# Kernel optimization log

Hardware: AMD Instinct MI355X
Metric: run time of the kernel (lower is better)

## Reference

```python
import jax, jax.numpy as jnp
import numpy as np

N = 100000   # nodes
D = 64       # in_features
E = 1200000  # edges (avg degree ~12)
C = 1.0      # curvature
MIN_NORM = 1e-15
PROJ_EPS = 4e-3  # float32 eps used by HGCN-style PoincareBall.proj


def setup_inputs() -> dict:
    key = jax.random.key(0)
    k1, k2, k3 = jax.random.split(key, 3)
    x = jax.random.normal(k1, (N, D), dtype=jnp.float32) * 0.1
    edge_index = jax.random.randint(k2, (2, E), 0, N, dtype=jnp.int32)
    # GCNConv learned params (lin weight + bias)
    W = jax.random.normal(k3, (D, D), dtype=jnp.float32) / np.sqrt(D)
    b = jnp.zeros((D,), dtype=jnp.float32)
    return {"x": x, "W": W, "b": b, "edge_index": edge_index}


def expmap0(u, c):
    sqrt_c = jnp.sqrt(c)
    u_norm = jnp.maximum(jnp.linalg.norm(u, axis=-1, keepdims=True), MIN_NORM)
    return jnp.tanh(sqrt_c * u_norm) * u / (sqrt_c * u_norm)


def proj(x, c):
    norm = jnp.maximum(jnp.linalg.norm(x, axis=-1, keepdims=True), MIN_NORM)
    maxnorm = (1.0 - PROJ_EPS) / jnp.sqrt(c)
    return jnp.where(norm > maxnorm, x / norm * maxnorm, x)


def gcn_conv(x, W, b, edge_index, n_nodes):
    # PyG GCNConv: h = x @ W; add self-loops; symmetric normalization; scatter-add; + bias
    h = x @ W  # [N, D]
    src, dst = edge_index[0], edge_index[1]
    loops = jnp.arange(n_nodes, dtype=edge_index.dtype)
    s = jnp.concatenate([src, loops])  # [E+N]
    d = jnp.concatenate([dst, loops])
    deg = jax.ops.segment_sum(jnp.ones(s.shape, dtype=h.dtype), d, num_segments=n_nodes)
    deg_inv_sqrt = jnp.where(deg > 0, deg ** -0.5, 0.0)
    norm = deg_inv_sqrt[s] * deg_inv_sqrt[d]  # [E+N]
    msgs = h[s] * norm[:, None]               # gather + scale: [E+N, D]
    out = jax.ops.segment_sum(msgs, d, num_segments=n_nodes)  # scatter-add
    return out + b


def reference(x, W, b, edge_index):
    # Note: original computes logmap0(x) but discards it (conv uses raw x) -- dead code.
    support_t = gcn_conv(x, W, b, edge_index, N)
    return proj(expmap0(support_t, C), C)
```

## Files before the change

kernel.cpp:

```cpp
#include <hip/hip_runtime.h>
#include <hip/hip_bf16.h>

#define DFEAT 64
#define NBSH  8
#define NPB   256
#define EPB   4096
#define EPT   (EPB / 256)
#define CAPB  3584
#define REGS  4608
#define BSTR  32

__global__ __launch_bounds__(256) void part_kernel(const int* __restrict__ ei,
                                                   int* __restrict__ bcnt,
                                                   unsigned* __restrict__ ebuf, int E) {
    __shared__ int h[512];
    __shared__ int base[512];
    int t = threadIdx.x;
    h[t] = 0; h[t + 256] = 0;
    __syncthreads();
    int bb = blockIdx.x * EPB;
    int sv[EPT], dv[EPT];
    #pragma unroll
    for (int i = 0; i < EPT; ++i) {
        int e = bb + i * 256 + t;
        if (e < E) {
            sv[i] = ei[e];
            dv[i] = ei[E + e];
            atomicAdd(&h[dv[i] >> NBSH], 1);
        } else dv[i] = -1;
    }
    __syncthreads();
    base[t]       = h[t]       ? atomicAdd(&bcnt[t * BSTR],         h[t])       : 0;
    base[t + 256] = h[t + 256] ? atomicAdd(&bcnt[(t + 256) * BSTR], h[t + 256]) : 0;
    __syncthreads();
    h[t] = 0; h[t + 256] = 0;
    __syncthreads();
    #pragma unroll
    for (int i = 0; i < EPT; ++i) {
        if (dv[i] >= 0) {
            int bkt = dv[i] >> NBSH;
            int pos = base[bkt] + atomicAdd(&h[bkt], 1);
            if (pos < CAPB)
                ebuf[(size_t)bkt * REGS + pos] =
                    (unsigned)sv[i] | ((unsigned)(dv[i] & (NPB - 1)) << 17);
        }
    }
}

__global__ __launch_bounds__(256) void csr_kernel(const int* __restrict__ bcnt,
                                                  unsigned* __restrict__ buf,
                                                  int2* __restrict__ bl,
                                                  float* __restrict__ dinv, int n) {
    __shared__ unsigned eb[CAPB];
    __shared__ int cnt[256];
    __shared__ int tmp[256];
    int t = threadIdx.x, b = blockIdx.x;
    int ecnt = bcnt[b * BSTR]; if (ecnt > CAPB) ecnt = CAPB;
    size_t rb = (size_t)b * REGS;

    const uint4* bufv = (const uint4*)(buf + rb);
    uint4* ebv = (uint4*)eb;
    int nv = (ecnt + 3) >> 2;
    for (int i = t; i < nv; i += 256) ebv[i] = bufv[i];
    cnt[t] = 0;
    __syncthreads();
    for (int i = t; i < ecnt; i += 256) atomicAdd(&cnt[eb[i] >> 17], 1);
    __syncthreads();

    int nid = (b << NBSH) + t;
    int deg = cnt[t];
    int slots = (nid < n) ? ((deg + 4) & ~3) : 0;
    tmp[t] = slots;
    __syncthreads();
    int s = slots;
    for (int o = 1; o < 256; o <<= 1) {
        int y = (t >= o) ? tmp[t - o] : 0;
        __syncthreads();
        tmp[t] += y;
        __syncthreads();
    }
    int excl = tmp[t] - s;
    int beg = (int)rb + excl;
    if (nid < n) {
        bl[nid] = make_int2(beg, slots);
        dinv[nid] = rsqrtf((float)(deg + 1));
        buf[beg] = (unsigned)nid;
        for (int k = deg + 1; k < slots; ++k) buf[beg + k] = (unsigned)n;
    }
    cnt[t] = excl + 1;
    __syncthreads();
    for (int i = t; i < ecnt; i += 256) {
        unsigned v = eb[i];
        int pos = atomicAdd(&cnt[v >> 17], 1);
        buf[rb + pos] = v & 0x1ffffu;
    }
}

__global__ __launch_bounds__(256) void xsprep_kernel(const float* __restrict__ x,
                                                     const float* __restrict__ dinv,
                                                     unsigned* __restrict__ xs, int n) {
    int i = blockIdx.x * blockDim.x + threadIdx.x;
    int total = (n + 1) * 32;
    if (i >= total) return;
    int row = i >> 5, col = i & 31;
    unsigned v = 0;
    if (row < n) {
        float di = dinv[row];
        float f0 = x[(size_t)row * DFEAT + 2 * col] * di;
        float f1 = x[(size_t)row * DFEAT + 2 * col + 1] * di;
        unsigned u0 = __float_as_uint(f0); u0 = (u0 + 0x7fffu + ((u0 >> 16) & 1u)) >> 16;
        unsigned u1 = __float_as_uint(f1); u1 = (u1 + 0x7fffu + ((u1 >> 16) & 1u)) >> 16;
        v = (u0 & 0xffffu) | (u1 << 16);
    }
    xs[i] = v;
}

__global__ __launch_bounds__(256) void agg_kernel(const int2* __restrict__ bl,
                                                  const int* __restrict__ srcs,
                                                  const float* __restrict__ dinv,
                                                  const uint2* __restrict__ xs2,
                                                  const float* __restrict__ W,
                                                  const float* __restrict__ b,
                                                  float* __restrict__ out,
                                                  int n, int octbase, int octend) {
    __shared__ float Wl[DFEAT * DFEAT];
    __shared__ float xl[8][DFEAT];
    int t = threadIdx.x;
    #pragma unroll
    for (int i = 0; i < 16; ++i) Wl[i * 256 + t] = W[i * 256 + t];
    __syncthreads();

    int r = t >> 6, lane = t & 63;
    int g = lane >> 4;
    int q = lane & 15;
    float bias = b[lane];

    for (int oct = octbase + blockIdx.x; oct < octend; oct += gridDim.x) {
        int na = oct * 8 + r;
        int nb_ = na + 4;
        bool va = na < n, vb = nb_ < n;
        if (!va) continue;

        int2 p0 = bl[na];
        int beg0 = p0.x, end0 = p0.x + p0.y;
        int beg1 = 0, end1 = 0;
        if (vb) { int2 p1 = bl[nb_]; beg1 = p1.x; end1 = p1.x + p1.y; }

        float a0 = 0, a1 = 0, a2 = 0, a3 = 0;
        float b0 = 0, b1 = 0, b2 = 0, b3 = 0;
        int base0 = beg0, base1 = beg1;
        while (base0 < end0 || base1 < end1) {
            int m0 = end0 - base0; m0 = m0 < 0 ? 0 : (m0 > 64 ? 64 : m0);
            int m1 = end1 - base1; m1 = m1 < 0 ? 0 : (m1 > 64 ? 64 : m1);
            int idx0 = 0, idx1 = 0;
            if (lane < m0) idx0 = srcs[base0 + lane];
            if (lane < m1) idx1 = srcs[base1 + lane];
            int q0 = m0 >> 2, q1 = m1 >> 2;
            int qc = q0 < q1 ? q0 : q1;
            #pragma unroll 4
            for (int j = 0; j < qc; ++j) {
                int sv0 = __shfl(idx0, 4 * j + g, 64);
                int sv1 = __shfl(idx1, 4 * j + g, 64);
                uint2 d0 = xs2[(unsigned)sv0 * 16 + q];
                uint2 d1 = xs2[(unsigned)sv1 * 16 + q];
                a0 += __uint_as_float(d0.x << 16);
                a1 += __uint_as_float(d0.x & 0xffff0000u);
                a2 += __uint_as_float(d0.y << 16);
                a3 += __uint_as_float(d0.y & 0xffff0000u);
                b0 += __uint_as_float(d1.x << 16);
                b1 += __uint_as_float(d1.x & 0xffff0000u);
                b2 += __uint_as_float(d1.y << 16);
                b3 += __uint_as_float(d1.y & 0xffff0000u);
            }
            #pragma unroll 4
            for (int j = qc; j < q0; ++j) {
                int sv0 = __shfl(idx0, 4 * j + g, 64);
                uint2 d0 = xs2[(unsigned)sv0 * 16 + q];
                a0 += __uint_as_float(d0.x << 16);
                a1 += __uint_as_float(d0.x & 0xffff0000u);
                a2 += __uint_as_float(d0.y << 16);
                a3 += __uint_as_float(d0.y & 0xffff0000u);
            }
            #pragma unroll 4
            for (int j = qc; j < q1; ++j) {
                int sv1 = __shfl(idx1, 4 * j + g, 64);
                uint2 d1 = xs2[(unsigned)sv1 * 16 + q];
                b0 += __uint_as_float(d1.x << 16);
                b1 += __uint_as_float(d1.x & 0xffff0000u);
                b2 += __uint_as_float(d1.y << 16);
                b3 += __uint_as_float(d1.y & 0xffff0000u);
            }
            base0 += 64; base1 += 64;
        }
        #pragma unroll
        for (int off = 16; off < 64; off <<= 1) {
            a0 += __shfl_xor(a0, off, 64);
            a1 += __shfl_xor(a1, off, 64);
            a2 += __shfl_xor(a2, off, 64);
            a3 += __shfl_xor(a3, off, 64);
            b0 += __shfl_xor(b0, off, 64);
            b1 += __shfl_xor(b1, off, 64);
            b2 += __shfl_xor(b2, off, 64);
            b3 += __shfl_xor(b3, off, 64);
        }
        if (g == 0) {
            float dia = dinv[na];
            xl[r][4 * q + 0] = a0 * dia;
            xl[r][4 * q + 1] = a1 * dia;
            xl[r][4 * q + 2] = a2 * dia;
            xl[r][4 * q + 3] = a3 * dia;
            if (vb) {
                float dib = dinv[nb_];
                xl[r + 4][4 * q + 0] = b0 * dib;
                xl[r + 4][4 * q + 1] = b1 * dib;
                xl[r + 4][4 * q + 2] = b2 * dib;
                xl[r + 4][4 * q + 3] = b3 * dib;
            }
        }

        float oa0 = bias, oa1 = 0.0f, ob0 = bias, ob1 = 0.0f;
        #pragma unroll
        for (int k = 0; k < DFEAT; k += 2) {
            float w0 = Wl[k * DFEAT + lane];
            float w1 = Wl[(k + 1) * DFEAT + lane];
            oa0 = fmaf(xl[r][k],     w0, oa0);
            oa1 = fmaf(xl[r][k + 1], w1, oa1);
            ob0 = fmaf(xl[r + 4][k],     w0, ob0);
            ob1 = fmaf(xl[r + 4][k + 1], w1, ob1);
        }
        float oa = oa0 + oa1;
        float ob = ob0 + ob1;

        float ssa = oa * oa, ssb = ob * ob;
        #pragma unroll
        for (int off = 32; off > 0; off >>= 1) {
            ssa += __shfl_xor(ssa, off, 64);
            ssb += __shfl_xor(ssb, off, 64);
        }
        float norma = fmaxf(sqrtf(ssa), 1e-15f);
        float sca = fminf(tanhf(norma), 1.0f - 4e-3f) / norma;
        out[(long long)na * DFEAT + lane] = oa * sca;
        if (vb) {
            float normb = fmaxf(sqrtf(ssb), 1e-15f);
            float scb = fminf(tanhf(normb), 1.0f - 4e-3f) / normb;
            out[(long long)nb_ * DFEAT + lane] = ob * scb;
        }
    }
}


extern "C" void kernel_launch(void* const* d_in, const int* in_sizes, int n_in,
                              void* d_out, int out_size, void* d_ws, size_t ws_size,
                              hipStream_t stream) {
    const float* x = (const float*)d_in[0];
    const float* W = (const float*)d_in[1];
    const float* b = (const float*)d_in[2];
    const int* ei  = (const int*)d_in[3];

    int n = in_sizes[0] / DFEAT;
    int E = in_sizes[3] / 2;
    int NBUCK = (n + NPB - 1) / NPB;
    int nblk = (E + EPB - 1) / EPB;
    int noctets = (n + 7) / 8;

    int* bcnt = (int*)d_ws;
    unsigned* buf = (unsigned*)(bcnt + 512 * BSTR);
    int2* bl = (int2*)(buf + (size_t)NBUCK * REGS);
    float* dinv = (float*)(bl + n);
    size_t xsoff = (size_t)(((int*)dinv + n) - (int*)d_ws);
    xsoff = (xsoff + 31) & ~(size_t)31;
    unsigned* xs = (unsigned*)d_ws + xsoff;

    float* out = (float*)d_out;

    int xsblocks = ((n + 1) * 32 + 255) / 256;

    hipMemsetAsync(bcnt, 0, 512 * BSTR * sizeof(int), stream);
    part_kernel  <<<nblk, 256, 0, stream>>>(ei, bcnt, buf, E);
    csr_kernel   <<<NBUCK, 256, 0, stream>>>(bcnt, buf, bl, dinv, n);
    xsprep_kernel<<<xsblocks, 256, 0, stream>>>(x, dinv, xs, n);

    int Q = (noctets + 3) / 4;
    for (int qd = 0; qd < 4; ++qd) {
        int ob = qd * Q;
        int oe = ob + Q; if (oe > noctets) oe = noctets;
        if (ob >= oe) break;
        int blks = oe - ob; if (blks > 2048) blks = 2048;
        agg_kernel<<<blks, 256, 0, stream>>>(bl, (const int*)buf, dinv,
                                             (const uint2*)xs, W, b, out, n, ob, oe);
    }
}
```

Baseline: 192.1 us.

## Fuse partition, CSR build, feature prep and aggregation into one cooperative kernel

```diff
diff --git a/kernel.cpp b/kernel.cpp
--- a/kernel.cpp
+++ b/kernel.cpp
@@ -1,5 +1,7 @@
 #include <hip/hip_runtime.h>
-#include <hip/hip_bf16.h>
+#include <hip/hip_cooperative_groups.h>
+
+namespace cg = cooperative_groups;
 
 #define DFEAT 64
 #define NBSH  8
@@ -9,241 +11,248 @@
 #define CAPB  3584
 #define REGS  4608
 #define BSTR  32
-
-__global__ __launch_bounds__(256) void part_kernel(const int* __restrict__ ei,
-                                                   int* __restrict__ bcnt,
-                                                   unsigned* __restrict__ ebuf, int E) {
-    __shared__ int h[512];
-    __shared__ int base[512];
+#define GRID  1024
+
+__global__ __launch_bounds__(256, 4) void mega_kernel(
+    const int* __restrict__ ei, const float* __restrict__ x,
+    const float* __restrict__ W, const float* __restrict__ bias_,
+    int* __restrict__ bcnt, unsigned* __restrict__ buf,
+    int2* __restrict__ bl, float* __restrict__ dinv,
+    unsigned* __restrict__ xs, float* __restrict__ out,
+    int n, int E, int nblk, int nbuck, int noctets)
+{
+    cg::grid_group grid = cg::this_grid();
+    __shared__ __align__(16) unsigned char smem[18432];
     int t = threadIdx.x;
-    h[t] = 0; h[t + 256] = 0;
-    __syncthreads();
-    int bb = blockIdx.x * EPB;
-    int sv[EPT], dv[EPT];
-    #pragma unroll
-    for (int i = 0; i < EPT; ++i) {
-        int e = bb + i * 256 + t;
-        if (e < E) {
-            sv[i] = ei[e];
-            dv[i] = ei[E + e];
-            atomicAdd(&h[dv[i] >> NBSH], 1);
-        } else dv[i] = -1;
-    }
-    __syncthreads();
-    base[t]       = h[t]       ? atomicAdd(&bcnt[t * BSTR],         h[t])       : 0;
-    base[t + 256] = h[t + 256] ? atomicAdd(&bcnt[(t + 256) * BSTR], h[t + 256]) : 0;
-    __syncthreads();
-    h[t] = 0; h[t + 256] = 0;
-    __syncthreads();
-    #pragma unroll
-    for (int i = 0; i < EPT; ++i) {
-        if (dv[i] >= 0) {
-            int bkt = dv[i] >> NBSH;
-            int pos = base[bkt] + atomicAdd(&h[bkt], 1);
-            if (pos < CAPB)
-                ebuf[(size_t)bkt * REGS + pos] =
-                    (unsigned)sv[i] | ((unsigned)(dv[i] & (NPB - 1)) << 17);
-        }
-    }
-}
-
-__global__ __launch_bounds__(256) void csr_kernel(const int* __restrict__ bcnt,
-                                                  unsigned* __restrict__ buf,
-                                                  int2* __restrict__ bl,
-                                                  float* __restrict__ dinv, int n) {
-    __shared__ unsigned eb[CAPB];
-    __shared__ int cnt[256];
-    __shared__ int tmp[256];
-    int t = threadIdx.x, b = blockIdx.x;
-    int ecnt = bcnt[b * BSTR]; if (ecnt > CAPB) ecnt = CAPB;
-    size_t rb = (size_t)b * REGS;
-
-    const uint4* bufv = (const uint4*)(buf + rb);
-    uint4* ebv = (uint4*)eb;
-    int nv = (ecnt + 3) >> 2;
-    for (int i = t; i < nv; i += 256) ebv[i] = bufv[i];
-    cnt[t] = 0;
-    __syncthreads();
-    for (int i = t; i < ecnt; i += 256) atomicAdd(&cnt[eb[i] >> 17], 1);
-    __syncthreads();
-
-    int nid = (b << NBSH) + t;
-    int deg = cnt[t];
-    int slots = (nid < n) ? ((deg + 4) & ~3) : 0;
-    tmp[t] = slots;
-    __syncthreads();
-    int s = slots;
-    for (int o = 1; o < 256; o <<= 1) {
-        int y = (t >= o) ? tmp[t - o] : 0;
-        __syncthreads();
-        tmp[t] += y;
-        __syncthreads();
-    }
-    int excl = tmp[t] - s;
-    int beg = (int)rb + excl;
-    if (nid < n) {
-        bl[nid] = make_int2(beg, slots);
-        dinv[nid] = rsqrtf((float)(deg + 1));
-        buf[beg] = (unsigned)nid;
-        for (int k = deg + 1; k < slots; ++k) buf[beg + k] = (unsigned)n;
-    }
-    cnt[t] = excl + 1;
-    __syncthreads();
-    for (int i = t; i < ecnt; i += 256) {
-        unsigned v = eb[i];
-        int pos = atomicAdd(&cnt[v >> 17], 1);
-        buf[rb + pos] = v & 0x1ffffu;
-    }
-}
-
-__global__ __launch_bounds__(256) void xsprep_kernel(const float* __restrict__ x,
-                                                     const float* __restrict__ dinv,
-                                                     unsigned* __restrict__ xs, int n) {
-    int i = blockIdx.x * blockDim.x + threadIdx.x;
-    int total = (n + 1) * 32;
-    if (i >= total) return;
-    int row = i >> 5, col = i & 31;
-    unsigned v = 0;
-    if (row < n) {
-        float di = dinv[row];
-        float f0 = x[(size_t)row * DFEAT + 2 * col] * di;
-        float f1 = x[(size_t)row * DFEAT + 2 * col + 1] * di;
-        unsigned u0 = __float_as_uint(f0); u0 = (u0 + 0x7fffu + ((u0 >> 16) & 1u)) >> 16;
-        unsigned u1 = __float_as_uint(f1); u1 = (u1 + 0x7fffu + ((u1 >> 16) & 1u)) >> 16;
-        v = (u0 & 0xffffu) | (u1 << 16);
-    }
-    xs[i] = v;
-}
-
-__global__ __launch_bounds__(256) void agg_kernel(const int2* __restrict__ bl,
-                                                  const int* __restrict__ srcs,
-                                                  const float* __restrict__ dinv,
-                                                  const uint2* __restrict__ xs2,
-                                                  const float* __restrict__ W,
-                                                  const float* __restrict__ b,
-                                                  float* __restrict__ out,
-                                                  int n, int octbase, int octend) {
-    __shared__ float Wl[DFEAT * DFEAT];
-    __shared__ float xl[8][DFEAT];
-    int t = threadIdx.x;
-    #pragma unroll
-    for (int i = 0; i < 16; ++i) Wl[i * 256 + t] = W[i * 256 + t];
-    __syncthreads();
-
-    int r = t >> 6, lane = t & 63;
-    int g = lane >> 4;
-    int q = lane & 15;
-    float bias = b[lane];
-
-    for (int oct = octbase + blockIdx.x; oct < octend; oct += gridDim.x) {
-        int na = oct * 8 + r;
-        int nb_ = na + 4;
-        bool va = na < n, vb = nb_ < n;
-        if (!va) continue;
-
-        int2 p0 = bl[na];
-        int beg0 = p0.x, end0 = p0.x + p0.y;
-        int beg1 = 0, end1 = 0;
-        if (vb) { int2 p1 = bl[nb_]; beg1 = p1.x; end1 = p1.x + p1.y; }
-
-        float a0 = 0, a1 = 0, a2 = 0, a3 = 0;
-        float b0 = 0, b1 = 0, b2 = 0, b3 = 0;
-        int base0 = beg0, base1 = beg1;
-        while (base0 < end0 || base1 < end1) {
-            int m0 = end0 - base0; m0 = m0 < 0 ? 0 : (m0 > 64 ? 64 : m0);
-            int m1 = end1 - base1; m1 = m1 < 0 ? 0 : (m1 > 64 ? 64 : m1);
-            int idx0 = 0, idx1 = 0;
-            if (lane < m0) idx0 = srcs[base0 + lane];
-            if (lane < m1) idx1 = srcs[base1 + lane];
-            int q0 = m0 >> 2, q1 = m1 >> 2;
-            int qc = q0 < q1 ? q0 : q1;
-            #pragma unroll 4
-            for (int j = 0; j < qc; ++j) {
-                int sv0 = __shfl(idx0, 4 * j + g, 64);
-                int sv1 = __shfl(idx1, 4 * j + g, 64);
-                uint2 d0 = xs2[(unsigned)sv0 * 16 + q];
-                uint2 d1 = xs2[(unsigned)sv1 * 16 + q];
-                a0 += __uint_as_float(d0.x << 16);
-                a1 += __uint_as_float(d0.x & 0xffff0000u);
-                a2 += __uint_as_float(d0.y << 16);
-                a3 += __uint_as_float(d0.y & 0xffff0000u);
-                b0 += __uint_as_float(d1.x << 16);
-                b1 += __uint_as_float(d1.x & 0xffff0000u);
-                b2 += __uint_as_float(d1.y << 16);
-                b3 += __uint_as_float(d1.y & 0xffff0000u);
-            }
-            #pragma unroll 4
-            for (int j = qc; j < q0; ++j) {
-                int sv0 = __shfl(idx0, 4 * j + g, 64);
-                uint2 d0 = xs2[(unsigned)sv0 * 16 + q];
-                a0 += __uint_as_float(d0.x << 16);
-                a1 += __uint_as_float(d0.x & 0xffff0000u);
-                a2 += __uint_as_float(d0.y << 16);
-                a3 += __uint_as_float(d0.y & 0xffff0000u);
-            }
-            #pragma unroll 4
-            for (int j = qc; j < q1; ++j) {
-                int sv1 = __shfl(idx1, 4 * j + g, 64);
-                uint2 d1 = xs2[(unsigned)sv1 * 16 + q];
-                b0 += __uint_as_float(d1.x << 16);
-                b1 += __uint_as_float(d1.x & 0xffff0000u);
-                b2 += __uint_as_float(d1.y << 16);
-                b3 += __uint_as_float(d1.y & 0xffff0000u);
-            }
-            base0 += 64; base1 += 64;
-        }
+    int bid = blockIdx.x;
+
+    for (int i = bid * 256 + t; i < 512 * BSTR; i += GRID * 256) bcnt[i] = 0;
+    grid.sync();
+
+    if (bid < nblk) {
+        int* h    = (int*)smem;
+        int* base = h + 512;
+        h[t] = 0; h[t + 256] = 0;
+        __syncthreads();
+        int bb = bid * EPB;
+        int sv[EPT], dv[EPT];
         #pragma unroll
-        for (int off = 16; off < 64; off <<= 1) {
-            a0 += __shfl_xor(a0, off, 64);
-            a1 += __shfl_xor(a1, off, 64);
-            a2 += __shfl_xor(a2, off, 64);
-            a3 += __shfl_xor(a3, off, 64);
-            b0 += __shfl_xor(b0, off, 64);
-            b1 += __shfl_xor(b1, off, 64);
-            b2 += __shfl_xor(b2, off, 64);
-            b3 += __shfl_xor(b3, off, 64);
-        }
-        if (g == 0) {
-            float dia = dinv[na];
-            xl[r][4 * q + 0] = a0 * dia;
-            xl[r][4 * q + 1] = a1 * dia;
-            xl[r][4 * q + 2] = a2 * dia;
-            xl[r][4 * q + 3] = a3 * dia;
+        for (int i = 0; i < EPT; ++i) {
+            int e = bb + i * 256 + t;
+            if (e < E) {
+                sv[i] = ei[e];
+                dv[i] = ei[E + e];
+                atomicAdd(&h[dv[i] >> NBSH], 1);
+            } else dv[i] = -1;
+        }
+        __syncthreads();
+        base[t]       = h[t]       ? atomicAdd(&bcnt[t * BSTR],         h[t])       : 0;
+        base[t + 256] = h[t + 256] ? atomicAdd(&bcnt[(t + 256) * BSTR], h[t + 256]) : 0;
+        __syncthreads();
+        h[t] = 0; h[t + 256] = 0;
+        __syncthreads();
+        #pragma unroll
+        for (int i = 0; i < EPT; ++i) {
+            if (dv[i] >= 0) {
+                int bkt = dv[i] >> NBSH;
+                int pos = base[bkt] + atomicAdd(&h[bkt], 1);
+                if (pos < CAPB)
+                    buf[(size_t)bkt * REGS + pos] =
+                        (unsigned)sv[i] | ((unsigned)(dv[i] & (NPB - 1)) << 17);
+            }
+        }
+    }
+    grid.sync();
+
+    if (bid < nbuck) {
+        unsigned* eb = (unsigned*)smem;
+        int* cnt = (int*)(smem + CAPB * 4);
+        int* tmp = cnt + 256;
+        int b = bid;
+        int ecnt = bcnt[b * BSTR]; if (ecnt > CAPB) ecnt = CAPB;
+        size_t rb = (size_t)b * REGS;
+
+        const uint4* bufv = (const uint4*)(buf + rb);
+        uint4* ebv = (uint4*)eb;
+        int nv = (ecnt + 3) >> 2;
+        for (int i = t; i < nv; i += 256) ebv[i] = bufv[i];
+        cnt[t] = 0;
+        __syncthreads();
+        for (int i = t; i < ecnt; i += 256) atomicAdd(&cnt[eb[i] >> 17], 1);
+        __syncthreads();
+
+        int nid = (b << NBSH) + t;
+        int deg = cnt[t];
+        int slots = (nid < n) ? ((deg + 4) & ~3) : 0;
+        tmp[t] = slots;
+        __syncthreads();
+        int s = slots;
+        for (int o = 1; o < 256; o <<= 1) {
+            int y = (t >= o) ? tmp[t - o] : 0;
+            __syncthreads();
+            tmp[t] += y;
+            __syncthreads();
+        }
+        int excl = tmp[t] - s;
+        int beg = (int)rb + excl;
+        if (nid < n) {
+            bl[nid] = make_int2(beg, slots);
+            dinv[nid] = rsqrtf((float)(deg + 1));
+            buf[beg] = (unsigned)nid;
+            for (int k = deg + 1; k < slots; ++k) buf[beg + k] = (unsigned)n;
+        }
+        cnt[t] = excl + 1;
+        __syncthreads();
+        for (int i = t; i < ecnt; i += 256) {
+            unsigned v = eb[i];
+            int pos = atomicAdd(&cnt[v >> 17], 1);
+            buf[rb + pos] = v & 0x1ffffu;
+        }
+    }
+    grid.sync();
+
+    {
+        int total = (n + 1) * 32;
+        for (int i = bid * 256 + t; i < total; i += GRID * 256) {
+            int row = i >> 5, col = i & 31;
+            unsigned v = 0;
+            if (row < n) {
+                float di = dinv[row];
+                float f0 = x[(size_t)row * DFEAT + 2 * col] * di;
+                float f1 = x[(size_t)row * DFEAT + 2 * col + 1] * di;
+                unsigned u0 = __float_as_uint(f0); u0 = (u0 + 0x7fffu + ((u0 >> 16) & 1u)) >> 16;
+                unsigned u1 = __float_as_uint(f1); u1 = (u1 + 0x7fffu + ((u1 >> 16) & 1u)) >> 16;
+                v = (u0 & 0xffffu) | (u1 << 16);
+            }
+            xs[i] = v;
+        }
+    }
+    grid.sync();
+
+    {
+        float* Wl = (float*)smem;
+        float (*xl)[DFEAT] = (float (*)[DFEAT])(smem + DFEAT * DFEAT * 4);
+        const uint2* xs2 = (const uint2*)xs;
+        const int* srcs = (const int*)buf;
+        #pragma unroll
+        for (int i = 0; i < 16; ++i) Wl[i * 256 + t] = W[i * 256 + t];
+        __syncthreads();
+
+        int r = t >> 6, lane = t & 63;
+        int g = lane >> 4;
+        int q = lane & 15;
+        float bias = bias_[lane];
+
+        for (int oct = bid; oct < noctets; oct += GRID) {
+            int na = oct * 8 + r;
+            int nb_ = na + 4;
+            bool va = na < n, vb = nb_ < n;
+            if (!va) continue;
+
+            int2 p0 = bl[na];
+            int beg0 = p0.x, end0 = p0.x + p0.y;
+            int beg1 = 0, end1 = 0;
+            if (vb) { int2 p1 = bl[nb_]; beg1 = p1.x; end1 = p1.x + p1.y; }
+
+            float a0 = 0, a1 = 0, a2 = 0, a3 = 0;
+            float b0 = 0, b1 = 0, b2 = 0, b3 = 0;
+            int base0 = beg0, base1 = beg1;
+            while (base0 < end0 || base1 < end1) {
+                int m0 = end0 - base0; m0 = m0 < 0 ? 0 : (m0 > 64 ? 64 : m0);
+                int m1 = end1 - base1; m1 = m1 < 0 ? 0 : (m1 > 64 ? 64 : m1);
+                int idx0 = 0, idx1 = 0;
+                if (lane < m0) idx0 = srcs[base0 + lane];
+                if (lane < m1) idx1 = srcs[base1 + lane];
+                int q0 = m0 >> 2, q1 = m1 >> 2;
+                int qc = q0 < q1 ? q0 : q1;
+                #pragma unroll 4
+                for (int j = 0; j < qc; ++j) {
+                    int sv0 = __shfl(idx0, 4 * j + g, 64);
+                    int sv1 = __shfl(idx1, 4 * j + g, 64);
+                    uint2 d0 = xs2[(unsigned)sv0 * 16 + q];
+                    uint2 d1 = xs2[(unsigned)sv1 * 16 + q];
+                    a0 += __uint_as_float(d0.x << 16);
+                    a1 += __uint_as_float(d0.x & 0xffff0000u);
+                    a2 += __uint_as_float(d0.y << 16);
+                    a3 += __uint_as_float(d0.y & 0xffff0000u);
+                    b0 += __uint_as_float(d1.x << 16);
+                    b1 += __uint_as_float(d1.x & 0xffff0000u);
+                    b2 += __uint_as_float(d1.y << 16);
+                    b3 += __uint_as_float(d1.y & 0xffff0000u);
+                }
+                #pragma unroll 4
+                for (int j = qc; j < q0; ++j) {
+                    int sv0 = __shfl(idx0, 4 * j + g, 64);
+                    uint2 d0 = xs2[(unsigned)sv0 * 16 + q];
+                    a0 += __uint_as_float(d0.x << 16);
+                    a1 += __uint_as_float(d0.x & 0xffff0000u);
+                    a2 += __uint_as_float(d0.y << 16);
+                    a3 += __uint_as_float(d0.y & 0xffff0000u);
+                }
+                #pragma unroll 4
+                for (int j = qc; j < q1; ++j) {
+                    int sv1 = __shfl(idx1, 4 * j + g, 64);
+                    uint2 d1 = xs2[(unsigned)sv1 * 16 + q];
+                    b0 += __uint_as_float(d1.x << 16);
+                    b1 += __uint_as_float(d1.x & 0xffff0000u);
+                    b2 += __uint_as_float(d1.y << 16);
+                    b3 += __uint_as_float(d1.y & 0xffff0000u);
+                }
+                base0 += 64; base1 += 64;
+            }
+            #pragma unroll
+            for (int off = 16; off < 64; off <<= 1) {
+                a0 += __shfl_xor(a0, off, 64);
+                a1 += __shfl_xor(a1, off, 64);
+                a2 += __shfl_xor(a2, off, 64);
+                a3 += __shfl_xor(a3, off, 64);
+                b0 += __shfl_xor(b0, off, 64);
+                b1 += __shfl_xor(b1, off, 64);
+                b2 += __shfl_xor(b2, off, 64);
+                b3 += __shfl_xor(b3, off, 64);
+            }
+            if (g == 0) {
+                float dia = dinv[na];
+                xl[r][4 * q + 0] = a0 * dia;
+                xl[r][4 * q + 1] = a1 * dia;
+                xl[r][4 * q + 2] = a2 * dia;
+                xl[r][4 * q + 3] = a3 * dia;
+                if (vb) {
+                    float dib = dinv[nb_];
+                    xl[r + 4][4 * q + 0] = b0 * dib;
+                    xl[r + 4][4 * q + 1] = b1 * dib;
+                    xl[r + 4][4 * q + 2] = b2 * dib;
+                    xl[r + 4][4 * q + 3] = b3 * dib;
+                }
+            }
+
+            float oa0 = bias, oa1 = 0.0f, ob0 = bias, ob1 = 0.0f;
+            #pragma unroll
+            for (int k = 0; k < DFEAT; k += 2) {
+                float w0 = Wl[k * DFEAT + lane];
+                float w1 = Wl[(k + 1) * DFEAT + lane];
+                oa0 = fmaf(xl[r][k],     w0, oa0);
+                oa1 = fmaf(xl[r][k + 1], w1, oa1);
+                ob0 = fmaf(xl[r + 4][k],     w0, ob0);
+                ob1 = fmaf(xl[r + 4][k + 1], w1, ob1);
+            }
+            float oa = oa0 + oa1;
+            float ob = ob0 + ob1;
+
+            float ssa = oa * oa, ssb = ob * ob;
+            #pragma unroll
+            for (int off = 32; off > 0; off >>= 1) {
+                ssa += __shfl_xor(ssa, off, 64);
+                ssb += __shfl_xor(ssb, off, 64);
+            }
+            float norma = fmaxf(sqrtf(ssa), 1e-15f);
+            float sca = fminf(tanhf(norma), 1.0f - 4e-3f) / norma;
+            out[(long long)na * DFEAT + lane] = oa * sca;
             if (vb) {
-                float dib = dinv[nb_];
-                xl[r + 4][4 * q + 0] = b0 * dib;
-                xl[r + 4][4 * q + 1] = b1 * dib;
-                xl[r + 4][4 * q + 2] = b2 * dib;
-                xl[r + 4][4 * q + 3] = b3 * dib;
-            }
-        }
-
-        float oa0 = bias, oa1 = 0.0f, ob0 = bias, ob1 = 0.0f;
-        #pragma unroll
-        for (int k = 0; k < DFEAT; k += 2) {
-            float w0 = Wl[k * DFEAT + lane];
-            float w1 = Wl[(k + 1) * DFEAT + lane];
-            oa0 = fmaf(xl[r][k],     w0, oa0);
-            oa1 = fmaf(xl[r][k + 1], w1, oa1);
-            ob0 = fmaf(xl[r + 4][k],     w0, ob0);
-            ob1 = fmaf(xl[r + 4][k + 1], w1, ob1);
-        }
-        float oa = oa0 + oa1;
-        float ob = ob0 + ob1;
-
-        float ssa = oa * oa, ssb = ob * ob;
-        #pragma unroll
-        for (int off = 32; off > 0; off >>= 1) {
-            ssa += __shfl_xor(ssa, off, 64);
-            ssb += __shfl_xor(ssb, off, 64);
-        }
-        float norma = fmaxf(sqrtf(ssa), 1e-15f);
-        float sca = fminf(tanhf(norma), 1.0f - 4e-3f) / norma;
-        out[(long long)na * DFEAT + lane] = oa * sca;
-        if (vb) {
-            float normb = fmaxf(sqrtf(ssb), 1e-15f);
-            float scb = fminf(tanhf(normb), 1.0f - 4e-3f) / normb;
-            out[(long long)nb_ * DFEAT + lane] = ob * scb;
+                float normb = fmaxf(sqrtf(ssb), 1e-15f);
+                float scb = fminf(tanhf(normb), 1.0f - 4e-3f) / normb;
+                out[(long long)nb_ * DFEAT + lane] = ob * scb;
+            }
         }
     }
 }
@@ -252,20 +261,20 @@
 extern "C" void kernel_launch(void* const* d_in, const int* in_sizes, int n_in,
                               void* d_out, int out_size, void* d_ws, size_t ws_size,
                               hipStream_t stream) {
+    const int* ei  = (const int*)d_in[3];
     const float* x = (const float*)d_in[0];
     const float* W = (const float*)d_in[1];
     const float* b = (const float*)d_in[2];
-    const int* ei  = (const int*)d_in[3];
 
     int n = in_sizes[0] / DFEAT;
     int E = in_sizes[3] / 2;
-    int NBUCK = (n + NPB - 1) / NPB;
+    int nbuck = (n + NPB - 1) / NPB;
     int nblk = (E + EPB - 1) / EPB;
     int noctets = (n + 7) / 8;
 
     int* bcnt = (int*)d_ws;
     unsigned* buf = (unsigned*)(bcnt + 512 * BSTR);
-    int2* bl = (int2*)(buf + (size_t)NBUCK * REGS);
+    int2* bl = (int2*)(buf + (size_t)nbuck * REGS);
     float* dinv = (float*)(bl + n);
     size_t xsoff = (size_t)(((int*)dinv + n) - (int*)d_ws);
     xsoff = (xsoff + 31) & ~(size_t)31;
@@ -273,20 +282,11 @@
 
     float* out = (float*)d_out;
 
-    int xsblocks = ((n + 1) * 32 + 255) / 256;
-
-    hipMemsetAsync(bcnt, 0, 512 * BSTR * sizeof(int), stream);
-    part_kernel  <<<nblk, 256, 0, stream>>>(ei, bcnt, buf, E);
-    csr_kernel   <<<NBUCK, 256, 0, stream>>>(bcnt, buf, bl, dinv, n);
-    xsprep_kernel<<<xsblocks, 256, 0, stream>>>(x, dinv, xs, n);
-
-    int Q = (noctets + 3) / 4;
-    for (int qd = 0; qd < 4; ++qd) {
-        int ob = qd * Q;
-        int oe = ob + Q; if (oe > noctets) oe = noctets;
-        if (ob >= oe) break;
-        int blks = oe - ob; if (blks > 2048) blks = 2048;
-        agg_kernel<<<blks, 256, 0, stream>>>(bl, (const int*)buf, dinv,
-                                             (const uint2*)xs, W, b, out, n, ob, oe);
-    }
+    void* args[] = { (void*)&ei, (void*)&x, (void*)&W, (void*)&b,
+                     (void*)&bcnt, (void*)&buf, (void*)&bl, (void*)&dinv,
+                     (void*)&xs, (void*)&out,
+                     (void*)&n, (void*)&E, (void*)&nblk, (void*)&nbuck, (void*)&noctets };
+
+    hipLaunchCooperativeKernel((const void*)mega_kernel, dim3(GRID), dim3(256),
+                               args, 0, stream);
 }
```

After: 585.3 us. +204.7%, slower.

## Process four nodes per wavefront and merge aggregation launches into one

Applied to the files above, without the earlier changes.

```diff
diff --git a/kernel.cpp b/kernel.cpp
--- a/kernel.cpp
+++ b/kernel.cpp
@@ -122,9 +122,9 @@
                                                   const float* __restrict__ W,
                                                   const float* __restrict__ b,
                                                   float* __restrict__ out,
-                                                  int n, int octbase, int octend) {
+                                                  int n, int nhex) {
     __shared__ float Wl[DFEAT * DFEAT];
-    __shared__ float xl[8][DFEAT];
+    __shared__ float xl[16][DFEAT];
     int t = threadIdx.x;
     #pragma unroll
     for (int i = 0; i < 16; ++i) Wl[i * 256 + t] = W[i * 256 + t];
@@ -135,115 +135,153 @@
     int q = lane & 15;
     float bias = b[lane];
 
-    for (int oct = octbase + blockIdx.x; oct < octend; oct += gridDim.x) {
-        int na = oct * 8 + r;
-        int nb_ = na + 4;
-        bool va = na < n, vb = nb_ < n;
-        if (!va) continue;
-
-        int2 p0 = bl[na];
-        int beg0 = p0.x, end0 = p0.x + p0.y;
-        int beg1 = 0, end1 = 0;
-        if (vb) { int2 p1 = bl[nb_]; beg1 = p1.x; end1 = p1.x + p1.y; }
+    for (int hx = blockIdx.x; hx < nhex; hx += gridDim.x) {
+        int n0 = hx * 16 + r;
+        int n1 = n0 + 4, n2 = n0 + 8, n3 = n0 + 12;
+        bool v0 = n0 < n, v1 = n1 < n, v2 = n2 < n, v3 = n3 < n;
+        if (!v0) continue;
+
+        int2 p = bl[n0];
+        int base0 = p.x, end0 = p.x + p.y;
+        int base1 = 0, end1 = 0, base2 = 0, end2 = 0, base3 = 0, end3 = 0;
+        if (v1) { int2 pp = bl[n1]; base1 = pp.x; end1 = pp.x + pp.y; }
+        if (v2) { int2 pp = bl[n2]; base2 = pp.x; end2 = pp.x + pp.y; }
+        if (v3) { int2 pp = bl[n3]; base3 = pp.x; end3 = pp.x + pp.y; }
 
         float a0 = 0, a1 = 0, a2 = 0, a3 = 0;
         float b0 = 0, b1 = 0, b2 = 0, b3 = 0;
-        int base0 = beg0, base1 = beg1;
-        while (base0 < end0 || base1 < end1) {
+        float c0 = 0, c1 = 0, c2 = 0, c3 = 0;
+        float d0_ = 0, d1_ = 0, d2_ = 0, d3_ = 0;
+
+        while (base0 < end0 || base1 < end1 || base2 < end2 || base3 < end3) {
             int m0 = end0 - base0; m0 = m0 < 0 ? 0 : (m0 > 64 ? 64 : m0);
             int m1 = end1 - base1; m1 = m1 < 0 ? 0 : (m1 > 64 ? 64 : m1);
-            int idx0 = 0, idx1 = 0;
-            if (lane < m0) idx0 = srcs[base0 + lane];
-            if (lane < m1) idx1 = srcs[base1 + lane];
-            int q0 = m0 >> 2, q1 = m1 >> 2;
-            int qc = q0 < q1 ? q0 : q1;
+            int m2 = end2 - base2; m2 = m2 < 0 ? 0 : (m2 > 64 ? 64 : m2);
+            int m3 = end3 - base3; m3 = m3 < 0 ? 0 : (m3 > 64 ? 64 : m3);
+            int i0 = 0, i1 = 0, i2 = 0, i3 = 0;
+            if (lane < m0) i0 = srcs[base0 + lane];
+            if (lane < m1) i1 = srcs[base1 + lane];
+            if (lane < m2) i2 = srcs[base2 + lane];
+            if (lane < m3) i3 = srcs[base3 + lane];
+            int q0 = m0 >> 2, q1 = m1 >> 2, q2 = m2 >> 2, q3 = m3 >> 2;
+            int qa = q0 > q1 ? q0 : q1;
+            int qb = q2 > q3 ? q2 : q3;
+            int qm = qa > qb ? qa : qb;
             #pragma unroll 4
-            for (int j = 0; j < qc; ++j) {
-                int sv0 = __shfl(idx0, 4 * j + g, 64);
-                int sv1 = __shfl(idx1, 4 * j + g, 64);
-                uint2 d0 = xs2[(unsigned)sv0 * 16 + q];
-                uint2 d1 = xs2[(unsigned)sv1 * 16 + q];
-                a0 += __uint_as_float(d0.x << 16);
-                a1 += __uint_as_float(d0.x & 0xffff0000u);
-                a2 += __uint_as_float(d0.y << 16);
-                a3 += __uint_as_float(d0.y & 0xffff0000u);
-                b0 += __uint_as_float(d1.x << 16);
-                b1 += __uint_as_float(d1.x & 0xffff0000u);
-                b2 += __uint_as_float(d1.y << 16);
-                b3 += __uint_as_float(d1.y & 0xffff0000u);
+            for (int j = 0; j < qm; ++j) {
+                if (j < q0) {
+                    int sv = __shfl(i0, 4 * j + g, 64);
+                    uint2 d = xs2[(unsigned)sv * 16 + q];
+                    a0 += __uint_as_float(d.x << 16);
+                    a1 += __uint_as_float(d.x & 0xffff0000u);
+                    a2 += __uint_as_float(d.y << 16);
+                    a3 += __uint_as_float(d.y & 0xffff0000u);
+                }
+                if (j < q1) {
+                    int sv = __shfl(i1, 4 * j + g, 64);
+                    uint2 d = xs2[(unsigned)sv * 16 + q];
+                    b0 += __uint_as_float(d.x << 16);
+                    b1 += __uint_as_float(d.x & 0xffff0000u);
+                    b2 += __uint_as_float(d.y << 16);
+                    b3 += __uint_as_float(d.y & 0xffff0000u);
+                }
+                if (j < q2) {
+                    int sv = __shfl(i2, 4 * j + g, 64);
+                    uint2 d = xs2[(unsigned)sv * 16 + q];
+                    c0 += __uint_as_float(d.x << 16);
+                    c1 += __uint_as_float(d.x & 0xffff0000u);
+                    c2 += __uint_as_float(d.y << 16);
+                    c3 += __uint_as_float(d.y & 0xffff0000u);
+                }
+                if (j < q3) {
+                    int sv = __shfl(i3, 4 * j + g, 64);
+                    uint2 d = xs2[(unsigned)sv * 16 + q];
+                    d0_ += __uint_as_float(d.x << 16);
+                    d1_ += __uint_as_float(d.x & 0xffff0000u);
+                    d2_ += __uint_as_float(d.y << 16);
+                    d3_ += __uint_as_float(d.y & 0xffff0000u);
+                }
             }
-            #pragma unroll 4
-            for (int j = qc; j < q0; ++j) {
-                int sv0 = __shfl(idx0, 4 * j + g, 64);
-                uint2 d0 = xs2[(unsigned)sv0 * 16 + q];
-                a0 += __uint_as_float(d0.x << 16);
-                a1 += __uint_as_float(d0.x & 0xffff0000u);
-                a2 += __uint_as_float(d0.y << 16);
-                a3 += __uint_as_float(d0.y & 0xffff0000u);
-            }
-            #pragma unroll 4
-            for (int j = qc; j < q1; ++j) {
-                int sv1 = __shfl(idx1, 4 * j + g, 64);
-                uint2 d1 = xs2[(unsigned)sv1 * 16 + q];
-                b0 += __uint_as_float(d1.x << 16);
-                b1 += __uint_as_float(d1.x & 0xffff0000u);
-                b2 += __uint_as_float(d1.y << 16);
-                b3 += __uint_as_float(d1.y & 0xffff0000u);
-            }
-            base0 += 64; base1 += 64;
+            base0 += 64; base1 += 64; base2 += 64; base3 += 64;
         }
         #pragma unroll
         for (int off = 16; off < 64; off <<= 1) {
-            a0 += __shfl_xor(a0, off, 64);
-            a1 += __shfl_xor(a1, off, 64);
-            a2 += __shfl_xor(a2, off, 64);
-            a3 += __shfl_xor(a3, off, 64);
-            b0 += __shfl_xor(b0, off, 64);
-            b1 += __shfl_xor(b1, off, 64);
-            b2 += __shfl_xor(b2, off, 64);
-            b3 += __shfl_xor(b3, off, 64);
+            a0 += __shfl_xor(a0, off, 64);  a1 += __shfl_xor(a1, off, 64);
+            a2 += __shfl_xor(a2, off, 64);  a3 += __shfl_xor(a3, off, 64);
+            b0 += __shfl_xor(b0, off, 64);  b1 += __shfl_xor(b1, off, 64);
+            b2 += __shfl_xor(b2, off, 64);  b3 += __shfl_xor(b3, off, 64);
+            c0 += __shfl_xor(c0, off, 64);  c1 += __shfl_xor(c1, off, 64);
+            c2 += __shfl_xor(c2, off, 64);  c3 += __shfl_xor(c3, off, 64);
+            d0_ += __shfl_xor(d0_, off, 64); d1_ += __shfl_xor(d1_, off, 64);
+            d2_ += __shfl_xor(d2_, off, 64); d3_ += __shfl_xor(d3_, off, 64);
         }
         if (g == 0) {
-            float dia = dinv[na];
-            xl[r][4 * q + 0] = a0 * dia;
-            xl[r][4 * q + 1] = a1 * dia;
-            xl[r][4 * q + 2] = a2 * dia;
-            xl[r][4 * q + 3] = a3 * dia;
-            if (vb) {
-                float dib = dinv[nb_];
-                xl[r + 4][4 * q + 0] = b0 * dib;
-                xl[r + 4][4 * q + 1] = b1 * dib;
-                xl[r + 4][4 * q + 2] = b2 * dib;
-                xl[r + 4][4 * q + 3] = b3 * dib;
+            float di0 = dinv[n0];
+            xl[r][4 * q + 0] = a0 * di0;
+            xl[r][4 * q + 1] = a1 * di0;
+            xl[r][4 * q + 2] = a2 * di0;
+            xl[r][4 * q + 3] = a3 * di0;
+            if (v1) {
+                float di1 = dinv[n1];
+                xl[r + 4][4 * q + 0] = b0 * di1;
+                xl[r + 4][4 * q + 1] = b1 * di1;
+                xl[r + 4][4 * q + 2] = b2 * di1;
+                xl[r + 4][4 * q + 3] = b3 * di1;
             }
-        }
-
-        float oa0 = bias, oa1 = 0.0f, ob0 = bias, ob1 = 0.0f;
+            if (v2) {
+                float di2 = dinv[n2];
+                xl[r + 8][4 * q + 0] = c0 * di2;
+                xl[r + 8][4 * q + 1] = c1 * di2;
+                xl[r + 8][4 * q + 2] = c2 * di2;
+                xl[r + 8][4 * q + 3] = c3 * di2;
+            }
+            if (v3) {
+                float di3 = dinv[n3];
+                xl[r + 12][4 * q + 0] = d0_ * di3;
+                xl[r + 12][4 * q + 1] = d1_ * di3;
+                xl[r + 12][4 * q + 2] = d2_ * di3;
+                xl[r + 12][4 * q + 3] = d3_ * di3;
+            }
+        }
+
+        float o0a = bias, o0b = 0.0f, o1a = bias, o1b = 0.0f;
+        float o2a = bias, o2b = 0.0f, o3a = bias, o3b = 0.0f;
         #pragma unroll
         for (int k = 0; k < DFEAT; k += 2) {
             float w0 = Wl[k * DFEAT + lane];
             float w1 = Wl[(k + 1) * DFEAT + lane];
-            oa0 = fmaf(xl[r][k],     w0, oa0);
-            oa1 = fmaf(xl[r][k + 1], w1, oa1);
-            ob0 = fmaf(xl[r + 4][k],     w0, ob0);
-            ob1 = fmaf(xl[r + 4][k + 1], w1, ob1);
-        }
-        float oa = oa0 + oa1;
-        float ob = ob0 + ob1;
-
-        float ssa = oa * oa, ssb = ob * ob;
+            o0a = fmaf(xl[r][k],          w0, o0a);
+            o0b = fmaf(xl[r][k + 1],      w1, o0b);
+            o1a = fmaf(xl[r + 4][k],      w0, o1a);
+            o1b = fmaf(xl[r + 4][k + 1],  w1, o1b);
+            o2a = fmaf(xl[r + 8][k],      w0, o2a);
+            o2b = fmaf(xl[r + 8][k + 1],  w1, o2b);
+            o3a = fmaf(xl[r + 12][k],     w0, o3a);
+            o3b = fmaf(xl[r + 12][k + 1], w1, o3b);
+        }
+        float o0 = o0a + o0b, o1 = o1a + o1b, o2 = o2a + o2b, o3 = o3a + o3b;
+
+        float s0 = o0 * o0, s1 = o1 * o1, s2 = o2 * o2, s3 = o3 * o3;
         #pragma unroll
         for (int off = 32; off > 0; off >>= 1) {
-            ssa += __shfl_xor(ssa, off, 64);
-            ssb += __shfl_xor(ssb, off, 64);
-        }
-        float norma = fmaxf(sqrtf(ssa), 1e-15f);
-        float sca = fminf(tanhf(norma), 1.0f - 4e-3f) / norma;
-        out[(long long)na * DFEAT + lane] = oa * sca;
-        if (vb) {
-            float normb = fmaxf(sqrtf(ssb), 1e-15f);
-            float scb = fminf(tanhf(normb), 1.0f - 4e-3f) / normb;
-            out[(long long)nb_ * DFEAT + lane] = ob * scb;
+            s0 += __shfl_xor(s0, off, 64);
+            s1 += __shfl_xor(s1, off, 64);
+            s2 += __shfl_xor(s2, off, 64);
+            s3 += __shfl_xor(s3, off, 64);
+        }
+        float nm0 = fmaxf(sqrtf(s0), 1e-15f);
+        out[(long long)n0 * DFEAT + lane] = o0 * (fminf(tanhf(nm0), 1.0f - 4e-3f) / nm0);
+        if (v1) {
+            float nm1 = fmaxf(sqrtf(s1), 1e-15f);
+            out[(long long)n1 * DFEAT + lane] = o1 * (fminf(tanhf(nm1), 1.0f - 4e-3f) / nm1);
+        }
+        if (v2) {
+            float nm2 = fmaxf(sqrtf(s2), 1e-15f);
+            out[(long long)n2 * DFEAT + lane] = o2 * (fminf(tanhf(nm2), 1.0f - 4e-3f) / nm2);
+        }
+        if (v3) {
+            float nm3 = fmaxf(sqrtf(s3), 1e-15f);
+            out[(long long)n3 * DFEAT + lane] = o3 * (fminf(tanhf(nm3), 1.0f - 4e-3f) / nm3);
         }
     }
 }
@@ -261,7 +299,7 @@
     int E = in_sizes[3] / 2;
     int NBUCK = (n + NPB - 1) / NPB;
     int nblk = (E + EPB - 1) / EPB;
-    int noctets = (n + 7) / 8;
+    int nhex = (n + 15) / 16;
 
     int* bcnt = (int*)d_ws;
     unsigned* buf = (unsigned*)(bcnt + 512 * BSTR);
@@ -273,20 +311,14 @@
 
     float* out = (float*)d_out;
 
+    int aggblocks = 2048;
+    if (aggblocks > nhex) aggblocks = nhex;
     int xsblocks = ((n + 1) * 32 + 255) / 256;
 
     hipMemsetAsync(bcnt, 0, 512 * BSTR * sizeof(int), stream);
     part_kernel  <<<nblk, 256, 0, stream>>>(ei, bcnt, buf, E);
     csr_kernel   <<<NBUCK, 256, 0, stream>>>(bcnt, buf, bl, dinv, n);
     xsprep_kernel<<<xsblocks, 256, 0, stream>>>(x, dinv, xs, n);
-
-    int Q = (noctets + 3) / 4;
-    for (int qd = 0; qd < 4; ++qd) {
-        int ob = qd * Q;
-        int oe = ob + Q; if (oe > noctets) oe = noctets;
-        if (ob >= oe) break;
-        int blks = oe - ob; if (blks > 2048) blks = 2048;
-        agg_kernel<<<blks, 256, 0, stream>>>(bl, (const int*)buf, dinv,
-                                             (const uint2*)xs, W, b, out, n, ob, oe);
-    }
-}
+    agg_kernel   <<<aggblocks, 256, 0, stream>>>(bl, (const int*)buf, dinv,
+                                                 (const uint2*)xs, W, b, out, n, nhex);
+}
```

New measurement: 186.4 us. -3.0%, faster.

## Gather 16-byte rows with 8 edges per wave-step and single agg launch

Applied to the files above, without the earlier changes.

```diff
diff --git a/kernel.cpp b/kernel.cpp
--- a/kernel.cpp
+++ b/kernel.cpp
@@ -7,8 +7,10 @@
 #define EPB   4096
 #define EPT   (EPB / 256)
 #define CAPB  3584
-#define REGS  4608
+#define REGS  5632
 #define BSTR  32
+
+typedef float f2 __attribute__((ext_vector_type(2)));
 
 __global__ __launch_bounds__(256) void part_kernel(const int* __restrict__ ei,
                                                    int* __restrict__ bcnt,
@@ -69,7 +71,7 @@
 
     int nid = (b << NBSH) + t;
     int deg = cnt[t];
-    int slots = (nid < n) ? ((deg + 4) & ~3) : 0;
+    int slots = (nid < n) ? ((deg + 8) & ~7) : 0;
     tmp[t] = slots;
     __syncthreads();
     int s = slots;
@@ -118,11 +120,11 @@
 __global__ __launch_bounds__(256) void agg_kernel(const int2* __restrict__ bl,
                                                   const int* __restrict__ srcs,
                                                   const float* __restrict__ dinv,
-                                                  const uint2* __restrict__ xs2,
+                                                  const uint4* __restrict__ xs4,
                                                   const float* __restrict__ W,
                                                   const float* __restrict__ b,
                                                   float* __restrict__ out,
-                                                  int n, int octbase, int octend) {
+                                                  int n, int noctets) {
     __shared__ float Wl[DFEAT * DFEAT];
     __shared__ float xl[8][DFEAT];
     int t = threadIdx.x;
@@ -131,105 +133,104 @@
     __syncthreads();
 
     int r = t >> 6, lane = t & 63;
-    int g = lane >> 4;
-    int q = lane & 15;
+    int g = lane >> 3;
+    int q = lane & 7;
     float bias = b[lane];
 
-    for (int oct = octbase + blockIdx.x; oct < octend; oct += gridDim.x) {
+    for (int oct = blockIdx.x; oct < noctets; oct += gridDim.x) {
         int na = oct * 8 + r;
         int nb_ = na + 4;
         bool va = na < n, vb = nb_ < n;
         if (!va) continue;
 
         int2 p0 = bl[na];
-        int beg0 = p0.x, end0 = p0.x + p0.y;
-        int beg1 = 0, end1 = 0;
-        if (vb) { int2 p1 = bl[nb_]; beg1 = p1.x; end1 = p1.x + p1.y; }
-
-        float a0 = 0, a1 = 0, a2 = 0, a3 = 0;
-        float b0 = 0, b1 = 0, b2 = 0, b3 = 0;
-        int base0 = beg0, base1 = beg1;
+        int base0 = p0.x, end0 = p0.x + p0.y;
+        int base1 = 0, end1 = 0;
+        if (vb) { int2 p1 = bl[nb_]; base1 = p1.x; end1 = p1.x + p1.y; }
+
+        float a0 = 0, a1 = 0, a2 = 0, a3 = 0, a4 = 0, a5 = 0, a6 = 0, a7 = 0;
+        float c0 = 0, c1 = 0, c2 = 0, c3 = 0, c4 = 0, c5 = 0, c6 = 0, c7 = 0;
         while (base0 < end0 || base1 < end1) {
             int m0 = end0 - base0; m0 = m0 < 0 ? 0 : (m0 > 64 ? 64 : m0);
             int m1 = end1 - base1; m1 = m1 < 0 ? 0 : (m1 > 64 ? 64 : m1);
             int idx0 = 0, idx1 = 0;
             if (lane < m0) idx0 = srcs[base0 + lane];
             if (lane < m1) idx1 = srcs[base1 + lane];
-            int q0 = m0 >> 2, q1 = m1 >> 2;
+            int q0 = m0 >> 3, q1 = m1 >> 3;
             int qc = q0 < q1 ? q0 : q1;
-            #pragma unroll 4
+            #pragma unroll 2
             for (int j = 0; j < qc; ++j) {
-                int sv0 = __shfl(idx0, 4 * j + g, 64);
-                int sv1 = __shfl(idx1, 4 * j + g, 64);
-                uint2 d0 = xs2[(unsigned)sv0 * 16 + q];
-                uint2 d1 = xs2[(unsigned)sv1 * 16 + q];
-                a0 += __uint_as_float(d0.x << 16);
-                a1 += __uint_as_float(d0.x & 0xffff0000u);
-                a2 += __uint_as_float(d0.y << 16);
-                a3 += __uint_as_float(d0.y & 0xffff0000u);
-                b0 += __uint_as_float(d1.x << 16);
-                b1 += __uint_as_float(d1.x & 0xffff0000u);
-                b2 += __uint_as_float(d1.y << 16);
-                b3 += __uint_as_float(d1.y & 0xffff0000u);
-            }
-            #pragma unroll 4
+                int sv0 = __shfl(idx0, 8 * j + g, 64);
+                int sv1 = __shfl(idx1, 8 * j + g, 64);
+                uint4 d0 = xs4[(unsigned)sv0 * 8 + q];
+                uint4 d1 = xs4[(unsigned)sv1 * 8 + q];
+                a0 += __uint_as_float(d0.x << 16); a1 += __uint_as_float(d0.x & 0xffff0000u);
+                a2 += __uint_as_float(d0.y << 16); a3 += __uint_as_float(d0.y & 0xffff0000u);
+                a4 += __uint_as_float(d0.z << 16); a5 += __uint_as_float(d0.z & 0xffff0000u);
+                a6 += __uint_as_float(d0.w << 16); a7 += __uint_as_float(d0.w & 0xffff0000u);
+                c0 += __uint_as_float(d1.x << 16); c1 += __uint_as_float(d1.x & 0xffff0000u);
+                c2 += __uint_as_float(d1.y << 16); c3 += __uint_as_float(d1.y & 0xffff0000u);
+                c4 += __uint_as_float(d1.z << 16); c5 += __uint_as_float(d1.z & 0xffff0000u);
+                c6 += __uint_as_float(d1.w << 16); c7 += __uint_as_float(d1.w & 0xffff0000u);
+            }
+            #pragma unroll 2
             for (int j = qc; j < q0; ++j) {
-                int sv0 = __shfl(idx0, 4 * j + g, 64);
-                uint2 d0 = xs2[(unsigned)sv0 * 16 + q];
-                a0 += __uint_as_float(d0.x << 16);
-                a1 += __uint_as_float(d0.x & 0xffff0000u);
-                a2 += __uint_as_float(d0.y << 16);
-                a3 += __uint_as_float(d0.y & 0xffff0000u);
-            }
-            #pragma unroll 4
+                int sv0 = __shfl(idx0, 8 * j + g, 64);
+                uint4 d0 = xs4[(unsigned)sv0 * 8 + q];
+                a0 += __uint_as_float(d0.x << 16); a1 += __uint_as_float(d0.x & 0xffff0000u);
+                a2 += __uint_as_float(d0.y << 16); a3 += __uint_as_float(d0.y & 0xffff0000u);
+                a4 += __uint_as_float(d0.z << 16); a5 += __uint_as_float(d0.z & 0xffff0000u);
+                a6 += __uint_as_float(d0.w << 16); a7 += __uint_as_float(d0.w & 0xffff0000u);
+            }
+            #pragma unroll 2
             for (int j = qc; j < q1; ++j) {
-                int sv1 = __shfl(idx1, 4 * j + g, 64);
-                uint2 d1 = xs2[(unsigned)sv1 * 16 + q];
-                b0 += __uint_as_float(d1.x << 16);
-                b1 += __uint_as_float(d1.x & 0xffff0000u);
-                b2 += __uint_as_float(d1.y << 16);
-                b3 += __uint_as_float(d1.y & 0xffff0000u);
+                int sv1 = __shfl(idx1, 8 * j + g, 64);
+                uint4 d1 = xs4[(unsigned)sv1 * 8 + q];
+                c0 += __uint_as_float(d1.x << 16); c1 += __uint_as_float(d1.x & 0xffff0000u);
+                c2 += __uint_as_float(d1.y << 16); c3 += __uint_as_float(d1.y & 0xffff0000u);
+                c4 += __uint_as_float(d1.z << 16); c5 += __uint_as_float(d1.z & 0xffff0000u);
+                c6 += __uint_as_float(d1.w << 16); c7 += __uint_as_float(d1.w & 0xffff0000u);
             }
             base0 += 64; base1 += 64;
         }
         #pragma unroll
-        for (int off = 16; off < 64; off <<= 1) {
-            a0 += __shfl_xor(a0, off, 64);
-            a1 += __shfl_xor(a1, off, 64);
-            a2 += __shfl_xor(a2, off, 64);
-            a3 += __shfl_xor(a3, off, 64);
-            b0 += __shfl_xor(b0, off, 64);
-            b1 += __shfl_xor(b1, off, 64);
-            b2 += __shfl_xor(b2, off, 64);
-            b3 += __shfl_xor(b3, off, 64);
+        for (int off = 8; off < 64; off <<= 1) {
+            a0 += __shfl_xor(a0, off, 64); a1 += __shfl_xor(a1, off, 64);
+            a2 += __shfl_xor(a2, off, 64); a3 += __shfl_xor(a3, off, 64);
+            a4 += __shfl_xor(a4, off, 64); a5 += __shfl_xor(a5, off, 64);
+            a6 += __shfl_xor(a6, off, 64); a7 += __shfl_xor(a7, off, 64);
+            c0 += __shfl_xor(c0, off, 64); c1 += __shfl_xor(c1, off, 64);
+            c2 += __shfl_xor(c2, off, 64); c3 += __shfl_xor(c3, off, 64);
+            c4 += __shfl_xor(c4, off, 64); c5 += __shfl_xor(c5, off, 64);
+            c6 += __shfl_xor(c6, off, 64); c7 += __shfl_xor(c7, off, 64);
         }
         if (g == 0) {
             float dia = dinv[na];
-            xl[r][4 * q + 0] = a0 * dia;
-            xl[r][4 * q + 1] = a1 * dia;
-            xl[r][4 * q + 2] = a2 * dia;
-            xl[r][4 * q + 3] = a3 * dia;
+            xl[r][8 * q + 0] = a0 * dia; xl[r][8 * q + 1] = a1 * dia;
+            xl[r][8 * q + 2] = a2 * dia; xl[r][8 * q + 3] = a3 * dia;
+            xl[r][8 * q + 4] = a4 * dia; xl[r][8 * q + 5] = a5 * dia;
+            xl[r][8 * q + 6] = a6 * dia; xl[r][8 * q + 7] = a7 * dia;
             if (vb) {
                 float dib = dinv[nb_];
-                xl[r + 4][4 * q + 0] = b0 * dib;
-                xl[r + 4][4 * q + 1] = b1 * dib;
-                xl[r + 4][4 * q + 2] = b2 * dib;
-                xl[r + 4][4 * q + 3] = b3 * dib;
-            }
-        }
-
-        float oa0 = bias, oa1 = 0.0f, ob0 = bias, ob1 = 0.0f;
+                xl[r + 4][8 * q + 0] = c0 * dib; xl[r + 4][8 * q + 1] = c1 * dib;
+                xl[r + 4][8 * q + 2] = c2 * dib; xl[r + 4][8 * q + 3] = c3 * dib;
+                xl[r + 4][8 * q + 4] = c4 * dib; xl[r + 4][8 * q + 5] = c5 * dib;
+                xl[r + 4][8 * q + 6] = c6 * dib; xl[r + 4][8 * q + 7] = c7 * dib;
+            }
+        }
+
+        f2 oA; oA.x = bias; oA.y = 0.0f;
+        f2 oB; oB.x = bias; oB.y = 0.0f;
         #pragma unroll
         for (int k = 0; k < DFEAT; k += 2) {
-            float w0 = Wl[k * DFEAT + lane];
-            float w1 = Wl[(k + 1) * DFEAT + lane];
-            oa0 = fmaf(xl[r][k],     w0, oa0);
-            oa1 = fmaf(xl[r][k + 1], w1, oa1);
-            ob0 = fmaf(xl[r + 4][k],     w0, ob0);
-            ob1 = fmaf(xl[r + 4][k + 1], w1, ob1);
-        }
-        float oa = oa0 + oa1;
-        float ob = ob0 + ob1;
+            f2 w; w.x = Wl[k * DFEAT + lane]; w.y = Wl[(k + 1) * DFEAT + lane];
+            f2 xa = *(const f2*)&xl[r][k];
+            f2 xb = *(const f2*)&xl[r + 4][k];
+            oA += xa * w;
+            oB += xb * w;
+        }
+        float oa = oA.x + oA.y;
+        float ob = oB.x + oB.y;
 
         float ssa = oa * oa, ssb = ob * ob;
         #pragma unroll
@@ -273,20 +274,14 @@
 
     float* out = (float*)d_out;
 
+    int aggblocks = 2048;
+    if (aggblocks > noctets) aggblocks = noctets;
     int xsblocks = ((n + 1) * 32 + 255) / 256;
 
     hipMemsetAsync(bcnt, 0, 512 * BSTR * sizeof(int), stream);
     part_kernel  <<<nblk, 256, 0, stream>>>(ei, bcnt, buf, E);
     csr_kernel   <<<NBUCK, 256, 0, stream>>>(bcnt, buf, bl, dinv, n);
     xsprep_kernel<<<xsblocks, 256, 0, stream>>>(x, dinv, xs, n);
-
-    int Q = (noctets + 3) / 4;
-    for (int qd = 0; qd < 4; ++qd) {
-        int ob = qd * Q;
-        int oe = ob + Q; if (oe > noctets) oe = noctets;
-        if (ob >= oe) break;
-        int blks = oe - ob; if (blks > 2048) blks = 2048;
-        agg_kernel<<<blks, 256, 0, stream>>>(bl, (const int*)buf, dinv,
-                                             (const uint2*)xs, W, b, out, n, ob, oe);
-    }
-}
+    agg_kernel   <<<aggblocks, 256, 0, stream>>>(bl, (const int*)buf, dinv,
+                                                 (const uint4*)xs, W, b, out, n, noctets);
+}
```

After: 195.6 us. Within noise of the previous version (+1.8%).
